# Kernel optimization log

Hardware: AMD Instinct MI355X
Metric: run time of the kernel (lower is better)

Reference implementation:

```python
import jax, jax.numpy as jnp
import numpy as np

TEMPERATURE = 1.0
NEG_BIG = -1.0e9


def _gumbel_softmax_hard(key, logits, temperature):
    # torch: rand_like().clamp(min=1e-10); -log(-log(u))
    u = jax.random.uniform(key, logits.shape, dtype=logits.dtype, minval=1e-10, maxval=1.0)
    g = -jnp.log(-jnp.log(u))
    y_soft = jax.nn.softmax((logits + g) / temperature, axis=-1)
    idx = jnp.argmax(y_soft, axis=-1)
    y_hard = jax.nn.one_hot(idx, logits.shape[-1], dtype=logits.dtype)
    # straight-through estimator
    return y_hard - jax.lax.stop_gradient(y_soft) + y_soft


def _eval_library(X, W1, b1, W2, b2):
    # X: (B, in_cols); W1: (M, in_cols, H); b1: (M, H); W2: (M, H); b2: (M,)
    h = jnp.tanh(jnp.einsum('bi,mih->mbh', X, W1) + b1[:, None, :])  # (M, B, H)
    return jnp.einsum('mbh,mh->bm', h, W2) + b2  # (B, M)


def setup_inputs() -> dict:
    key = jax.random.key(0)
    ks = jax.random.split(key, 8)
    B, S, M, H, IC, K = 32768, 2, 64, 128, 2, 2
    return {
        'X': jax.random.normal(ks[0], (B, IC), jnp.float32),
        'W1': jax.random.normal(ks[1], (M, IC, H), jnp.float32) * 0.3,
        'b1': jax.random.normal(ks[2], (M, H), jnp.float32) * 0.1,
        'W2': jax.random.normal(ks[3], (M, H), jnp.float32) * 0.3,
        'b2': jax.random.normal(ks[4], (M,), jnp.float32) * 0.1,
        'routers': jax.random.normal(ks[5], (S, M), jnp.float32),
        'coefficients': jax.random.normal(ks[6], (S, K, M), jnp.float32),
        'complexity_prior': jnp.zeros((M,), jnp.float32),
    }


def reference(X, W1, b1, W2, b2, routers, coefficients, complexity_prior):
    batch = X.shape[0]
    state_dim, k, n_mlps = coefficients.shape
    mlp_out = _eval_library(X, W1, b1, W2, b2)  # (B, M)

    gkey = jax.random.key(42)
    dXdt_pred, all_gates = [], []
    for d in range(state_dim):
        base_logits = jnp.broadcast_to((routers[d] + complexity_prior)[None, :], (batch, n_mlps))
        mask = jnp.zeros((batch, n_mlps), X.dtype)
        dxdt_d = jnp.zeros((batch,), X.dtype)
        slot_gates = []
        for j in range(k):
            kj = jax.random.fold_in(gkey, d * k + j)
            gate_j = _gumbel_softmax_hard(kj, base_logits + mask, TEMPERATURE)
            slot_gates.append(gate_j)
            mask = mask + NEG_BIG * jax.lax.stop_gradient(gate_j)
            dxdt_d = dxdt_d + jnp.sum(gate_j * coefficients[d, j][None, :] * mlp_out, axis=1)
        all_gates.append(jnp.stack(slot_gates, axis=0))  # (k, B, M)
        dXdt_pred.append(dxdt_d)
    return jnp.stack(dXdt_pred, axis=1), jnp.stack(all_gates, axis=0)
```

## Files before the change

### kernel.cpp

```cpp
#include <hip/hip_runtime.h>
#include <stdint.h>

#define BATCH 32768
#define NM 64

struct Keys { uint32_t k[8]; };

__host__ __device__ inline void threefry2x32(uint32_t k0, uint32_t k1,
                                             uint32_t x0, uint32_t x1,
                                             uint32_t* o0, uint32_t* o1) {
  uint32_t k2 = k0 ^ k1 ^ 0x1BD11BDAu;
  x0 += k0; x1 += k1;
#define TF_RND(r) { x0 += x1; x1 = (x1 << (r)) | (x1 >> (32 - (r))); x1 ^= x0; }
  TF_RND(13) TF_RND(15) TF_RND(26) TF_RND(6)
  x0 += k1; x1 += k2 + 1u;
  TF_RND(17) TF_RND(29) TF_RND(16) TF_RND(24)
  x0 += k2; x1 += k0 + 2u;
  TF_RND(13) TF_RND(15) TF_RND(26) TF_RND(6)
  x0 += k0; x1 += k1 + 3u;
  TF_RND(17) TF_RND(29) TF_RND(16) TF_RND(24)
  x0 += k1; x1 += k2 + 4u;
  TF_RND(13) TF_RND(15) TF_RND(26) TF_RND(6)
  x0 += k2; x1 += k0 + 5u;
#undef TF_RND
  *o0 = x0; *o1 = x1;
}

__device__ inline float gumbel_g(uint32_t bits) {
  float f = __uint_as_float((bits >> 9) | 0x3F800000u) - 1.0f;
  float u = fmaxf(1e-10f, f + 1e-10f);
  return -logf(-logf(u));
}

__device__ inline float tanh_fast(float x) {
  float e = __expf(2.0f * x);
#if __has_builtin(__builtin_amdgcn_rcpf)
  float r = __builtin_amdgcn_rcpf(e + 1.0f);
#else
  float r = 1.0f / (e + 1.0f);
#endif
  return fmaf(-2.0f, r, 1.0f);
}

__global__ __launch_bounds__(256) void k_fused(Keys keys,
    const float* __restrict__ X,   const float* __restrict__ W1,
    const float* __restrict__ b1v, const float* __restrict__ W2,
    const float* __restrict__ b2v, const float* __restrict__ routers,
    const float* __restrict__ coef, const float* __restrict__ cp,
    float* __restrict__ out0, float4* __restrict__ gates) {
  __shared__ float basev[2][NM];
  __shared__ float xlds[16 * 2];
  __shared__ float part[64];
  __shared__ uint8_t wlds[4][16];

  const int t = threadIdx.x;
  const int b0 = blockIdx.x * 16;

  if (t < 128) basev[t >> 6][t & 63] = routers[t] + cp[t & 63];
  if (t < 32)  xlds[t] = X[b0 * 2 + t];
  __syncthreads();

  const int g = t >> 2, sub = t & 3;
  const int dj = g & 3, bl = g >> 2;
  const uint32_t k0 = keys.k[dj * 2 + 0], k1 = keys.k[dj * 2 + 1];
  const uint32_t ibase = (uint32_t)(b0 + bl) * NM + (uint32_t)sub * 16;
  const float4* bq = (const float4*)&basev[dj >> 1][sub * 16];
  const float4 q0 = bq[0], q1 = bq[1], q2 = bq[2], q3 = bq[3];
  const float bvr[16] = {q0.x, q0.y, q0.z, q0.w, q1.x, q1.y, q1.z, q1.w,
                         q2.x, q2.y, q2.z, q2.w, q3.x, q3.y, q3.z, q3.w};
  float best = -1e30f, second = -1e30f;
  int bi = 0, si = 0;
#pragma unroll
  for (int mm = 0; mm < 16; ++mm) {
    uint32_t o0, o1;
    threefry2x32(k0, k1, 0u, ibase + (uint32_t)mm, &o0, &o1);
    float z = bvr[mm] + gumbel_g(o0 ^ o1);
    int m = sub * 16 + mm;
    if (z > best)        { second = best; si = bi; best = z; bi = m; }
    else if (z > second) { second = z; si = m; }
  }
#pragma unroll
  for (int dlt = 1; dlt <= 2; dlt <<= 1) {
    float ob = __shfl_xor(best, dlt);  int obi = __shfl_xor(bi, dlt);
    float os = __shfl_xor(second, dlt); int osi = __shfl_xor(si, dlt);
    bool selfWins = (best > ob) || (best == ob && bi < obi);
    if (selfWins) {
      if (ob > second || (ob == second && obi < si)) { second = ob; si = obi; }
    } else {
      if (best > os || (best == os && bi < osi)) { second = best; si = bi; }
      else { second = os; si = osi; }
      best = ob; bi = obi;
    }
  }
  const int w0p = __shfl_xor(bi, 4);
  const int w = ((g & 1) == 0) ? bi : ((bi == w0p) ? si : bi);
  if (sub == 0) wlds[dj][bl] = (uint8_t)w;
  __syncthreads();

  {
    const int gb = t >> 4, q = t & 15;
    const int m0 = q * 4;
#pragma unroll
    for (int it = 0; it < 4; ++it) {
      const int gw = wlds[it][gb];
      float4 v;
      v.x = (m0 + 0 == gw) ? 1.0f : 0.0f;
      v.y = (m0 + 1 == gw) ? 1.0f : 0.0f;
      v.z = (m0 + 2 == gw) ? 1.0f : 0.0f;
      v.w = (m0 + 3 == gw) ? 1.0f : 0.0f;
      gates[(it * BATCH + b0 + gb) * 16 + q] = v;
    }
  }

  const int wv = t >> 6, lane = t & 63;
  const int grp = lane >> 4, sl = lane & 15;
#pragma unroll
  for (int i = 0; i < 4; ++i) {
    const int r = wv * 16 + i * 4 + grp;
    const int rbl = r >> 2, rdj = r & 3;
    const int rw = wlds[rdj][rbl];
    const float xa = xlds[rbl * 2 + 0], xb = xlds[rbl * 2 + 1];
    const float4* A0 = (const float4*)(W1 + rw * 256 + sl * 8);
    const float4* A1 = (const float4*)(W1 + rw * 256 + 128 + sl * 8);
    const float4* B1 = (const float4*)(b1v + rw * 128 + sl * 8);
    const float4* WW = (const float4*)(W2 + rw * 128 + sl * 8);
    const float4 a0a = A0[0], a0b = A0[1];
    const float4 a1a = A1[0], a1b = A1[1];
    const float4 b1a = B1[0], b1b = B1[1];
    float h0 = fmaf(xb, a1a.x, fmaf(xa, a0a.x, b1a.x));
    float h1 = fmaf(xb, a1a.y, fmaf(xa, a0a.y, b1a.y));
    float h2 = fmaf(xb, a1a.z, fmaf(xa, a0a.z, b1a.z));
    float h3 = fmaf(xb, a1a.w, fmaf(xa, a0a.w, b1a.w));
    float h4 = fmaf(xb, a1b.x, fmaf(xa, a0b.x, b1b.x));
    float h5 = fmaf(xb, a1b.y, fmaf(xa, a0b.y, b1b.y));
    float h6 = fmaf(xb, a1b.z, fmaf(xa, a0b.z, b1b.z));
    float h7 = fmaf(xb, a1b.w, fmaf(xa, a0b.w, b1b.w));
    const float4 w2a = WW[0], w2b = WW[1];
    float s = tanh_fast(h0) * w2a.x;
    s = fmaf(tanh_fast(h1), w2a.y, s);
    s = fmaf(tanh_fast(h2), w2a.z, s);
    s = fmaf(tanh_fast(h3), w2a.w, s);
    s = fmaf(tanh_fast(h4), w2b.x, s);
    s = fmaf(tanh_fast(h5), w2b.y, s);
    s = fmaf(tanh_fast(h6), w2b.z, s);
    s = fmaf(tanh_fast(h7), w2b.w, s);
#pragma unroll
    for (int sft = 1; sft < 16; sft <<= 1) s += __shfl_xor(s, sft);
    if (sl == 0) part[r] = coef[rdj * NM + rw] * (s + b2v[rw]);
  }
  __syncthreads();

  if (t < 32) {
    const int obl = t >> 1, od = t & 1;
    out0[(b0 + obl) * 2 + od] =
        part[obl * 4 + od * 2 + 0] + part[obl * 4 + od * 2 + 1];
  }
}

extern "C" void kernel_launch(void* const* d_in, const int* in_sizes, int n_in,
                              void* d_out, int out_size, void* d_ws, size_t ws_size,
                              hipStream_t stream) {
  const float* X       = (const float*)d_in[0];
  const float* W1      = (const float*)d_in[1];
  const float* b1v     = (const float*)d_in[2];
  const float* W2      = (const float*)d_in[3];
  const float* b2v     = (const float*)d_in[4];
  const float* routers = (const float*)d_in[5];
  const float* coef    = (const float*)d_in[6];
  const float* cp      = (const float*)d_in[7];
  float* out0  = (float*)d_out;
  float* gates = out0 + BATCH * 2;

  Keys keys;
  for (uint32_t dj = 0; dj < 4; ++dj) {
    uint32_t o0, o1;
    threefry2x32(0u, 42u, 0u, dj, &o0, &o1);
    keys.k[dj * 2 + 0] = o0;
    keys.k[dj * 2 + 1] = o1;
  }

  k_fused<<<dim3(BATCH / 16), dim3(256), 0, stream>>>(
      keys, X, W1, b1v, W2, b2v, routers, coef, cp, out0, (float4*)gates);
}
```

Measured before the change: 35.69 us.

## Use cheap approximate Gumbel for top-3 screening, exact recompute for winners

Replaces the precise double logf Gumbel transform in the main 16-element scan with fast __logf plus a series for u near 1, tracking the top three candidates. Only the top two candidates are recomputed with the exact transform to decide the winner. When the second and third approximate values fall within a small margin, the wave falls back to the full exact scan. This aims to cut transcendental cost in the RNG-heavy selection phase, at the cost of an extra threefry per thread, more shuffles, and a divergent fallback path.

```diff
diff --git a/kernel.cpp b/kernel.cpp
--- a/kernel.cpp
+++ b/kernel.cpp
@@ -3,6 +3,7 @@
 
 #define BATCH 32768
 #define NM 64
+#define MARG 2e-4f
 
 struct Keys { uint32_t k[8]; };
 
@@ -32,6 +33,16 @@
   return -logf(-logf(u));
 }
 
+__device__ inline float gumbel_cheap(uint32_t bits) {
+  float f = __uint_as_float((bits >> 9) | 0x3F800000u) - 1.0f;
+  float u = fmaxf(1e-10f, f + 1e-10f);
+  float w = 1.0f - u;
+  float t_log = -__logf(u);
+  float t_ser = w * fmaf(w, fmaf(w, fmaf(w, 0.25f, 0.33333334f), 0.5f), 1.0f);
+  float t = (w <= 0.03125f) ? t_ser : t_log;
+  return -__logf(t);
+}
+
 __device__ inline float tanh_fast(float x) {
   float e = __expf(2.0f * x);
 #if __has_builtin(__builtin_amdgcn_rcpf)
@@ -63,38 +74,87 @@
   const int g = t >> 2, sub = t & 3;
   const int dj = g & 3, bl = g >> 2;
   const uint32_t k0 = keys.k[dj * 2 + 0], k1 = keys.k[dj * 2 + 1];
-  const uint32_t ibase = (uint32_t)(b0 + bl) * NM + (uint32_t)sub * 16;
+  const uint32_t rowbase = (uint32_t)(b0 + bl) * NM;
+  const uint32_t ibase = rowbase + (uint32_t)sub * 16;
   const float4* bq = (const float4*)&basev[dj >> 1][sub * 16];
   const float4 q0 = bq[0], q1 = bq[1], q2 = bq[2], q3 = bq[3];
   const float bvr[16] = {q0.x, q0.y, q0.z, q0.w, q1.x, q1.y, q1.z, q1.w,
                          q2.x, q2.y, q2.z, q2.w, q3.x, q3.y, q3.z, q3.w};
-  float best = -1e30f, second = -1e30f;
-  int bi = 0, si = 0;
+
+  float z1 = -1e30f, z2 = -1e30f, z3 = -1e30f;
+  int i1 = 0, i2 = 0;
 #pragma unroll
   for (int mm = 0; mm < 16; ++mm) {
     uint32_t o0, o1;
     threefry2x32(k0, k1, 0u, ibase + (uint32_t)mm, &o0, &o1);
-    float z = bvr[mm] + gumbel_g(o0 ^ o1);
+    float zc = bvr[mm] + gumbel_cheap(o0 ^ o1);
     int m = sub * 16 + mm;
-    if (z > best)        { second = best; si = bi; best = z; bi = m; }
-    else if (z > second) { second = z; si = m; }
+    if (zc > z1)      { z3 = z2; z2 = z1; i2 = i1; z1 = zc; i1 = m; }
+    else if (zc > z2) { z3 = z2; z2 = zc; i2 = m; }
+    else if (zc > z3) { z3 = zc; }
   }
 #pragma unroll
   for (int dlt = 1; dlt <= 2; dlt <<= 1) {
-    float ob = __shfl_xor(best, dlt);  int obi = __shfl_xor(bi, dlt);
-    float os = __shfl_xor(second, dlt); int osi = __shfl_xor(si, dlt);
-    bool selfWins = (best > ob) || (best == ob && bi < obi);
-    if (selfWins) {
-      if (ob > second || (ob == second && obi < si)) { second = ob; si = obi; }
-    } else {
-      if (best > os || (best == os && bi < osi)) { second = best; si = bi; }
-      else { second = os; si = osi; }
-      best = ob; bi = obi;
+    float oz1 = __shfl_xor(z1, dlt); int oi1 = __shfl_xor(i1, dlt);
+    float oz2 = __shfl_xor(z2, dlt); int oi2 = __shfl_xor(i2, dlt);
+    float oz3 = __shfl_xor(z3, dlt);
+    bool afirst = (z1 > oz1) || (z1 == oz1 && i1 < oi1);
+    float w1z = afirst ? z1 : oz1;  int w1i = afirst ? i1 : oi1;
+    float l1z = afirst ? oz1 : z1;  int l1i = afirst ? oi1 : i1;
+    float wz2 = afirst ? z2 : oz2;  int wi2 = afirst ? i2 : oi2;
+    float lz2 = afirst ? oz2 : z2;
+    float wz3 = afirst ? z3 : oz3;
+    bool lfirst = (l1z > wz2) || (l1z == wz2 && l1i < wi2);
+    float n2z = lfirst ? l1z : wz2; int n2i = lfirst ? l1i : wi2;
+    float n3z = lfirst ? fmaxf(wz2, lz2) : fmaxf(l1z, wz3);
+    z1 = w1z; i1 = w1i; z2 = n2z; i2 = n2i; z3 = n3z;
+  }
+
+  const int ci = (sub & 2) ? i2 : i1;
+  {
+    uint32_t o0, o1;
+    threefry2x32(k0, k1, 0u, rowbase + (uint32_t)ci, &o0, &o1);
+    float ze = basev[dj >> 1][ci] + gumbel_g(o0 ^ o1);
+    const int bl4 = (t & 63) & ~3;
+    float z1e = __shfl(ze, bl4);
+    float z2e = __shfl(ze, bl4 + 2);
+    bool c1w = (z1e > z2e) || (z1e == z2e && i1 < i2);
+    int best_i = c1w ? i1 : i2;
+    int sec_i  = c1w ? i2 : i1;
+
+    bool bad = (z3 > z2 - MARG);
+    if (__any(bad)) {
+      float eb = -1e30f, es = -1e30f;
+      int ebi = 0, esi = 0;
+#pragma unroll
+      for (int mm = 0; mm < 16; ++mm) {
+        uint32_t p0, p1;
+        threefry2x32(k0, k1, 0u, ibase + (uint32_t)mm, &p0, &p1);
+        float z = bvr[mm] + gumbel_g(p0 ^ p1);
+        int m = sub * 16 + mm;
+        if (z > eb)      { es = eb; esi = ebi; eb = z; ebi = m; }
+        else if (z > es) { es = z; esi = m; }
+      }
+#pragma unroll
+      for (int dlt = 1; dlt <= 2; dlt <<= 1) {
+        float ob = __shfl_xor(eb, dlt);  int obi = __shfl_xor(ebi, dlt);
+        float os = __shfl_xor(es, dlt);  int osi = __shfl_xor(esi, dlt);
+        bool selfWins = (eb > ob) || (eb == ob && ebi < obi);
+        if (selfWins) {
+          if (ob > es || (ob == es && obi < esi)) { es = ob; esi = obi; }
+        } else {
+          if (eb > os || (eb == os && ebi < osi)) { es = eb; esi = ebi; }
+          else { es = os; esi = osi; }
+          eb = ob; ebi = obi;
+        }
+      }
+      if (bad) { best_i = ebi; sec_i = esi; }
     }
-  }
-  const int w0p = __shfl_xor(bi, 4);
-  const int w = ((g & 1) == 0) ? bi : ((bi == w0p) ? si : bi);
-  if (sub == 0) wlds[dj][bl] = (uint8_t)w;
+
+    const int w0p = __shfl_xor(best_i, 4);
+    const int w = ((g & 1) == 0) ? best_i : ((best_i == w0p) ? sec_i : best_i);
+    if (sub == 0) wlds[dj][bl] = (uint8_t)w;
+  }
   __syncthreads();
 
   {
```

Result: slower. 39.36 us (+10.3%).

## Make each wavefront self-contained, replacing LDS and barriers with cross-lane shuffles

Applied to the files above, without the earlier changes.

Each 64-lane wavefront now owns 4 batch rows end to end. Router bias, X and expert choices come from direct global loads and wave shuffles instead of shared memory. All three __syncthreads and the shared-memory staging are gone, and the final pair reduction is done with a shuffle that writes out0 directly. This removes barrier stalls between the sampling, gate-write and MLP phases. The cost is redundant per-wave global loads of the router and X values.

```diff
diff --git a/kernel.cpp b/kernel.cpp
--- a/kernel.cpp
+++ b/kernel.cpp
@@ -48,26 +48,24 @@
     const float* __restrict__ b2v, const float* __restrict__ routers,
     const float* __restrict__ coef, const float* __restrict__ cp,
     float* __restrict__ out0, float4* __restrict__ gates) {
-  __shared__ float basev[2][NM];
-  __shared__ float xlds[16 * 2];
-  __shared__ float part[64];
-  __shared__ uint8_t wlds[4][16];
+  const int t = threadIdx.x;
+  const int wv = t >> 6, lane = t & 63;
+  const int b0w = blockIdx.x * 16 + wv * 4;
 
-  const int t = threadIdx.x;
-  const int b0 = blockIdx.x * 16;
-
-  if (t < 128) basev[t >> 6][t & 63] = routers[t] + cp[t & 63];
-  if (t < 32)  xlds[t] = X[b0 * 2 + t];
-  __syncthreads();
-
-  const int g = t >> 2, sub = t & 3;
+  const int g = lane >> 2, sub = lane & 3;
   const int dj = g & 3, bl = g >> 2;
   const uint32_t k0 = keys.k[dj * 2 + 0], k1 = keys.k[dj * 2 + 1];
-  const uint32_t ibase = (uint32_t)(b0 + bl) * NM + (uint32_t)sub * 16;
-  const float4* bq = (const float4*)&basev[dj >> 1][sub * 16];
-  const float4 q0 = bq[0], q1 = bq[1], q2 = bq[2], q3 = bq[3];
-  const float bvr[16] = {q0.x, q0.y, q0.z, q0.w, q1.x, q1.y, q1.z, q1.w,
-                         q2.x, q2.y, q2.z, q2.w, q3.x, q3.y, q3.z, q3.w};
+  const uint32_t ibase = (uint32_t)(b0w + bl) * NM + (uint32_t)sub * 16;
+
+  const float4* rq = (const float4*)(routers + (dj >> 1) * NM + sub * 16);
+  const float4* cq = (const float4*)(cp + sub * 16);
+  const float4 r0 = rq[0], r1 = rq[1], r2 = rq[2], r3 = rq[3];
+  const float4 c0 = cq[0], c1 = cq[1], c2 = cq[2], c3 = cq[3];
+  const float bvr[16] = {r0.x + c0.x, r0.y + c0.y, r0.z + c0.z, r0.w + c0.w,
+                         r1.x + c1.x, r1.y + c1.y, r1.z + c1.z, r1.w + c1.w,
+                         r2.x + c2.x, r2.y + c2.y, r2.z + c2.z, r2.w + c2.w,
+                         r3.x + c3.x, r3.y + c3.y, r3.z + c3.z, r3.w + c3.w};
+
   float best = -1e30f, second = -1e30f;
   int bi = 0, si = 0;
 #pragma unroll
@@ -94,39 +92,41 @@
   }
   const int w0p = __shfl_xor(bi, 4);
   const int w = ((g & 1) == 0) ? bi : ((bi == w0p) ? si : bi);
-  if (sub == 0) wlds[dj][bl] = (uint8_t)w;
-  __syncthreads();
 
   {
-    const int gb = t >> 4, q = t & 15;
+    const int gb = lane >> 4, q = lane & 15;
     const int m0 = q * 4;
 #pragma unroll
     for (int it = 0; it < 4; ++it) {
-      const int gw = wlds[it][gb];
+      const int gw = __shfl(w, (gb * 4 + it) * 4);
       float4 v;
       v.x = (m0 + 0 == gw) ? 1.0f : 0.0f;
       v.y = (m0 + 1 == gw) ? 1.0f : 0.0f;
       v.z = (m0 + 2 == gw) ? 1.0f : 0.0f;
       v.w = (m0 + 3 == gw) ? 1.0f : 0.0f;
-      gates[(it * BATCH + b0 + gb) * 16 + q] = v;
+      gates[((size_t)it * BATCH + b0w + gb) * 16 + q] = v;
     }
   }
 
-  const int wv = t >> 6, lane = t & 63;
   const int grp = lane >> 4, sl = lane & 15;
+  const char* W1b = (const char*)W1;
+  const char* B1b = (const char*)b1v;
+  const char* W2b = (const char*)W2;
 #pragma unroll
   for (int i = 0; i < 4; ++i) {
-    const int r = wv * 16 + i * 4 + grp;
-    const int rbl = r >> 2, rdj = r & 3;
-    const int rw = wlds[rdj][rbl];
-    const float xa = xlds[rbl * 2 + 0], xb = xlds[rbl * 2 + 1];
-    const float4* A0 = (const float4*)(W1 + rw * 256 + sl * 8);
-    const float4* A1 = (const float4*)(W1 + rw * 256 + 128 + sl * 8);
-    const float4* B1 = (const float4*)(b1v + rw * 128 + sl * 8);
-    const float4* WW = (const float4*)(W2 + rw * 128 + sl * 8);
-    const float4 a0a = A0[0], a0b = A0[1];
-    const float4 a1a = A1[0], a1b = A1[1];
-    const float4 b1a = B1[0], b1b = B1[1];
+    const int rw = __shfl(w, (i * 4 + grp) * 4);
+    const int brow = b0w + i;
+    const float xa = X[brow * 2 + 0], xb = X[brow * 2 + 1];
+    const int off  = (rw << 10) + (sl << 5);
+    const int off2 = (rw << 9)  + (sl << 5);
+    const float4 a0a = *(const float4*)(W1b + off);
+    const float4 a0b = *(const float4*)(W1b + off + 16);
+    const float4 a1a = *(const float4*)(W1b + off + 512);
+    const float4 a1b = *(const float4*)(W1b + off + 528);
+    const float4 b1a = *(const float4*)(B1b + off2);
+    const float4 b1b = *(const float4*)(B1b + off2 + 16);
+    const float4 w2a = *(const float4*)(W2b + off2);
+    const float4 w2b = *(const float4*)(W2b + off2 + 16);
     float h0 = fmaf(xb, a1a.x, fmaf(xa, a0a.x, b1a.x));
     float h1 = fmaf(xb, a1a.y, fmaf(xa, a0a.y, b1a.y));
     float h2 = fmaf(xb, a1a.z, fmaf(xa, a0a.z, b1a.z));
@@ -135,7 +135,6 @@
     float h5 = fmaf(xb, a1b.y, fmaf(xa, a0b.y, b1b.y));
     float h6 = fmaf(xb, a1b.z, fmaf(xa, a0b.z, b1b.z));
     float h7 = fmaf(xb, a1b.w, fmaf(xa, a0b.w, b1b.w));
-    const float4 w2a = WW[0], w2b = WW[1];
     float s = tanh_fast(h0) * w2a.x;
     s = fmaf(tanh_fast(h1), w2a.y, s);
     s = fmaf(tanh_fast(h2), w2a.z, s);
@@ -146,14 +145,10 @@
     s = fmaf(tanh_fast(h7), w2b.w, s);
 #pragma unroll
     for (int sft = 1; sft < 16; sft <<= 1) s += __shfl_xor(s, sft);
-    if (sl == 0) part[r] = coef[rdj * NM + rw] * (s + b2v[rw]);
-  }
-  __syncthreads();
-
-  if (t < 32) {
-    const int obl = t >> 1, od = t & 1;
-    out0[(b0 + obl) * 2 + od] =
-        part[obl * 4 + od * 2 + 0] + part[obl * 4 + od * 2 + 1];
+    const float val = coef[grp * NM + rw] * (s + b2v[rw]);
+    const float pv = __shfl_xor(val, 16);
+    if ((grp & 1) == 0 && sl == 0)
+      out0[brow * 2 + (grp >> 1)] = val + pv;
   }
 }
 
```

Result: no change. 35.35 us (-1.0%).
